# Kernel optimization log

Measured on AMD Instinct MI355X. Metric: run time of the kernel, lower is better.

The kernel has to match this reference:

```python
import jax, jax.numpy as jnp
import numpy as np

S, A, F, L, NCONV = 16, 512, 64, 12, 3


def setup_inputs() -> dict:
    key = jax.random.key(0)
    k1, k2, k3, k4 = jax.random.split(key, 4)
    node = jax.random.normal(k1, (S, A, F), dtype=jnp.float32)
    conn = jax.random.uniform(k2, (S, A, A, L), dtype=jnp.float32)
    bond = jax.random.normal(k3, (S, A, L, 2), dtype=jnp.float32)
    # filters.data.normal_() * (1/in_depth/1000) per ChemConv.__init__
    filters = jax.random.normal(k4, (NCONV, F, L, F + 2), dtype=jnp.float32) / (F * 1000.0)
    return {
        "node_property_tensor": node,
        "connectivity_tensor": conn,
        "bond_property_tensor": bond,
        "filters": filters,
    }


def _chemconv(x, conn, bond, w):
    # x: (S,A,F); conn: (S,A,A,L); bond: (S,A,L,2); w: (O,L,F+2)
    # gather neighbor features: bmm of (S,A,L,A) x (S,A,F) -> (S,A,L,F)
    ncv = jnp.einsum('sakl,skf->salf', conn, x)
    combined = jnp.concatenate([ncv, bond], axis=-1)  # (S,A,L,F+2)
    # elementwise-mul + double-sum == contraction over (L, F+2)
    return jnp.einsum('salc,olc->sao', combined, w)  # (S,A,O)


def reference(node_property_tensor, connectivity_tensor, bond_property_tensor, filters):
    out = node_property_tensor
    for i in range(filters.shape[0]):
        w = filters[i]  # same conv layer applied twice per residual pair
        out = jax.nn.relu(_chemconv(out, connectivity_tensor, bond_property_tensor, w))
        out = _chemconv(out, connectivity_tensor, bond_property_tensor, w)
        out = out + node_property_tensor  # residual to block input
        out = jax.nn.relu(out)
    return out
```

## Files before the change

kernel.cpp:

```cpp
#include <hip/hip_runtime.h>


typedef __attribute__((ext_vector_type(8))) short bf16x8;
typedef __attribute__((ext_vector_type(4))) float f32x4;
typedef unsigned short u16;
typedef unsigned int u32;
typedef unsigned char u8;
typedef long i64t;

#define YSCALE 16384.0f
#define YINV   (1.0f / 16384.0f)

__device__ __forceinline__ u16 f2bf(float f) {
  union { float f; u32 u; } x; x.f = f;
  u32 r = x.u + 0x7fffu + ((x.u >> 16) & 1u);
  return (u16)(r >> 16);
}

__device__ __forceinline__ u32 fp8pk4(float a, float b, float c, float d) {
  u32 w = __builtin_amdgcn_cvt_pk_fp8_f32(a, b, 0u, false);
  return __builtin_amdgcn_cvt_pk_fp8_f32(c, d, w, true);
}
__device__ __forceinline__ u32 fp8one(float v) {
  return __builtin_amdgcn_cvt_pk_fp8_f32(v, v, 0u, false) & 0xffu;
}

__device__ __forceinline__ void gload16(const void* g, void* l) {
  __builtin_amdgcn_global_load_lds((const __attribute__((address_space(1))) u32*)g,
                                   (__attribute__((address_space(3))) u32*)l, 16, 0, 0);
}

__global__ __launch_bounds__(256) void k_prep(const float* __restrict__ conn,
                                              const float* __restrict__ filters,
                                              const float* __restrict__ bond,
                                              u8* __restrict__ connQ,
                                              u16* __restrict__ wA,
                                              float* __restrict__ bW) {
  const int bid = blockIdx.x, tid = threadIdx.x;
  if (bid < 2048) {
    const unsigned n8 = 6291456u, stride = 2048 * 256;
    for (unsigned j = bid * 256 + tid; j < n8; j += stride) {
      const float4* s4 = (const float4*)conn;
      float4 a = s4[2 * (size_t)j], b = s4[2 * (size_t)j + 1];
      uint2 w;
      w.x = fp8pk4(a.x, a.y, a.z, a.w);
      w.y = fp8pk4(b.x, b.y, b.z, b.w);
      ((uint2*)connQ)[j] = w;
    }
  } else if (bid < 2624) {
    int t = (bid - 2048) * 256 + tid;
    int i = t / 49152;
    int rem = t - i * 49152;
    int row = rem >> 6, f = rem & 63;
    int l = row >> 6, o = row & 63;
    wA[t] = f2bf(filters[((size_t)((i * 64 + o) * 12 + l)) * 66 + f]);
  } else {
    __shared__ float wb[4608];
    __shared__ float lb[16 * 24];
    const int sa0 = (bid - 2624) * 16;
    for (int idx = tid; idx < 4608; idx += 256) {
      int i = idx / 1536, rem = idx - i * 1536;
      int o = rem / 24, lj = rem - o * 24;
      wb[idx] = filters[((size_t)((i * 64 + o) * 12 + (lj >> 1))) * 66 + 64 + (lj & 1)];
    }
    for (int t = tid; t < 384; t += 256)
      lb[t] = bond[(size_t)sa0 * 24 + t];
    __syncthreads();
#pragma unroll
    for (int it = 0; it < 12; ++it) {
      int idx = it * 256 + tid;
      int sl = idx / 192, rem = idx - sl * 192;
      int i = rem >> 6, o = rem & 63;
      float acc = 0.f;
#pragma unroll
      for (int lj = 0; lj < 24; ++lj)
        acc += lb[sl * 24 + lj] * wb[i * 1536 + o * 24 + lj];
      bW[(size_t)i * 524288 + (size_t)(sa0 + sl) * 64 + o] = acc;
    }
  }
}

__global__ __launch_bounds__(256) void k_yT(const float* __restrict__ node,
                                            const float* __restrict__ pOut,
                                            const float* __restrict__ bias,
                                            const u16* __restrict__ wAf,
                                            u8* __restrict__ yT,
                                            int mode, int addNode) {
  const int s = blockIdx.y, k0 = blockIdx.x * 32;
  __shared__ u16 xld[32 * 64];
  __shared__ u16 Z[12 * 64 * 36];
  const int tid = threadIdx.x, lane = tid & 63, wid = tid >> 6;
  const int r = lane & 15, g = lane >> 4;

  {
    const int row = tid >> 3, f0 = (tid & 7) * 8;
    const size_t e = ((size_t)(s * 512) + k0 + row) * 64 + f0;
    float v[8];
    if (mode == 0) {
      float4 a = *(const float4*)&node[e], b = *(const float4*)&node[e + 4];
      v[0] = a.x; v[1] = a.y; v[2] = a.z; v[3] = a.w;
      v[4] = b.x; v[5] = b.y; v[6] = b.z; v[7] = b.w;
    } else {
      float4 sa = {0, 0, 0, 0}, sb = {0, 0, 0, 0};
#pragma unroll
      for (int q = 0; q < 4; ++q) {
        float4 a = *(const float4*)&pOut[(size_t)q * 524288 + e];
        float4 b = *(const float4*)&pOut[(size_t)q * 524288 + e + 4];
        sa.x += a.x; sa.y += a.y; sa.z += a.z; sa.w += a.w;
        sb.x += b.x; sb.y += b.y; sb.z += b.z; sb.w += b.w;
      }
      float4 ba = *(const float4*)&bias[e], bb = *(const float4*)&bias[e + 4];
      sa.x = sa.x * YINV + ba.x; sa.y = sa.y * YINV + ba.y;
      sa.z = sa.z * YINV + ba.z; sa.w = sa.w * YINV + ba.w;
      sb.x = sb.x * YINV + bb.x; sb.y = sb.y * YINV + bb.y;
      sb.z = sb.z * YINV + bb.z; sb.w = sb.w * YINV + bb.w;
      if (addNode) {
        float4 na = *(const float4*)&node[e], nb = *(const float4*)&node[e + 4];
        sa.x += na.x; sa.y += na.y; sa.z += na.z; sa.w += na.w;
        sb.x += nb.x; sb.y += nb.y; sb.z += nb.z; sb.w += nb.w;
      }
      v[0] = fmaxf(sa.x, 0.f); v[1] = fmaxf(sa.y, 0.f);
      v[2] = fmaxf(sa.z, 0.f); v[3] = fmaxf(sa.w, 0.f);
      v[4] = fmaxf(sb.x, 0.f); v[5] = fmaxf(sb.y, 0.f);
      v[6] = fmaxf(sb.z, 0.f); v[7] = fmaxf(sb.w, 0.f);
    }
    ushort4 h0, h1;
    h0.x = f2bf(v[0]); h0.y = f2bf(v[1]); h0.z = f2bf(v[2]); h0.w = f2bf(v[3]);
    h1.x = f2bf(v[4]); h1.y = f2bf(v[5]); h1.z = f2bf(v[6]); h1.w = f2bf(v[7]);
    const int slot = (f0 >> 3) ^ (row & 7);
    *(ushort4*)&xld[row * 64 + slot * 8] = h0;
    *(ushort4*)&xld[row * 64 + slot * 8 + 4] = h1;
  }
  __syncthreads();

#pragma unroll
  for (int lw = 0; lw < 3; ++lw) {
    const int l = wid * 3 + lw;
    f32x4 acc[4][2] = {};
#pragma unroll
    for (int ks = 0; ks < 2; ++ks) {
      bf16x8 bv[2];
#pragma unroll
      for (int kt = 0; kt < 2; ++kt) {
        const int kk = kt * 16 + r;
        bv[kt] = *(const bf16x8*)&xld[kk * 64 + (((ks * 4 + g) ^ (kk & 7)) << 3)];
      }
#pragma unroll
      for (int ot = 0; ot < 4; ++ot) {
        bf16x8 av = *(const bf16x8*)&wAf[(size_t)(l * 64 + ot * 16 + r) * 64 + ks * 32 + g * 8];
#pragma unroll
        for (int kt = 0; kt < 2; ++kt)
          acc[ot][kt] = __builtin_amdgcn_mfma_f32_16x16x32_bf16(av, bv[kt], acc[ot][kt], 0, 0, 0);
      }
    }
#pragma unroll
    for (int ot = 0; ot < 4; ++ot)
#pragma unroll
      for (int kt = 0; kt < 2; ++kt)
#pragma unroll
        for (int r2 = 0; r2 < 4; ++r2) {
          int o = ot * 16 + g * 4 + r2, k = kt * 16 + r;
          Z[l * 2304 + o * 36 + k] = (u16)fp8one(acc[ot][kt][r2] * YSCALE);
        }
  }
  __syncthreads();
  u8* yb = yT + (size_t)s * 393216;
#pragma unroll
  for (int it = 0; it < 8; ++it) {
    int idx = it * 256 + tid;
    int o = idx >> 5, k = idx & 31;
    u32 b[12];
#pragma unroll
    for (int l = 0; l < 12; ++l) b[l] = (u32)(Z[l * 2304 + o * 36 + k] & 0xffu);
    u32* dst = (u32*)&yb[(size_t)o * 6144 + (size_t)(k0 + k) * 12];
    dst[0] = b[0] | (b[1] << 8) | (b[2] << 16) | (b[3] << 24);
    dst[1] = b[4] | (b[5] << 8) | (b[6] << 16) | (b[7] << 24);
    dst[2] = b[8] | (b[9] << 8) | (b[10] << 16) | (b[11] << 24);
  }
}

__global__ __launch_bounds__(512, 2) void k_stageB(const u8* __restrict__ connQ,
                                                   const u8* __restrict__ yT,
                                                   float* __restrict__ pOut) {
  const int b = blockIdx.x;
  const int s = (b & 7) * 2 + ((b >> 3) & 1);
  const int mt = (b >> 4) & 7, kq = b >> 7;
  const int row0 = mt * 64, k0 = kq * 1536;
  const u8* Ab = connQ + (size_t)(s * 512 + row0) * 6144 + k0;
  const u8* Bb = yT + (size_t)(s * 64) * 6144 + k0;
  __shared__ __align__(16) u8 lds[3 * 2 * 4096];
  const int tid = threadIdx.x, lane = tid & 63, wid = tid >> 6;
  const int r = lane & 15, g = lane >> 4;
  const int wr = wid & 3, wc = wid >> 2;
  const int isA = wid < 4;
  const int wseg = (isA ? wid : wid - 4) * 16;
  const u8* sbase = isA ? Ab : Bb;
  const int lrow = lane >> 2, lslot = lane & 3;
  const int side = isA ? 0 : 1;
  f32x4 acc[2] = {};

#define STAGE(T, NB)                                                            \
  {                                                                             \
    const int row = wseg + lrow;                                                \
    const int slot = lslot ^ ((row ^ (row >> 2)) & 3);                          \
    gload16(sbase + (size_t)row * 6144 + (size_t)(T) * 64 + slot * 16,          \
            &lds[((NB) * 2 + side) * 4096 + wseg * 64]);                        \
  }

  STAGE(0, 0);
  STAGE(1, 1);
  int nb = 0;
  for (int t = 0; t < 24; ++t) {
    if (t < 23) { asm volatile("s_waitcnt vmcnt(1)" ::: "memory"); }
    else        { asm volatile("s_waitcnt vmcnt(0)" ::: "memory"); }
    __builtin_amdgcn_s_barrier();
    if (t + 2 < 24) {
      int nb2 = nb + 2; if (nb2 >= 3) nb2 -= 3;
      STAGE(t + 2, nb2);
    }
    {
      const u8* bufA = &lds[(nb * 2 + 0) * 4096];
      const u8* bufB = &lds[(nb * 2 + 1) * 4096];
      const int arow = wr * 16 + r;
      const int ax = (arow ^ (arow >> 2)) & 3;
#pragma unroll
      for (int ks = 0; ks < 2; ++ks) {
        i64t av = *(const i64t*)&bufA[arow * 64 + (((ks * 2 + (g >> 1)) ^ ax) << 4) + ((g & 1) << 3)];
#pragma unroll
        for (int c = 0; c < 2; ++c) {
          const int col = wc * 32 + c * 16 + r;
          const int bx = (col ^ (col >> 2)) & 3;
          i64t bv = *(const i64t*)&bufB[col * 64 + (((ks * 2 + (g >> 1)) ^ bx) << 4) + ((g & 1) << 3)];
          acc[c] = __builtin_amdgcn_mfma_f32_16x16x32_fp8_fp8(av, bv, acc[c], 0, 0, 0);
        }
      }
    }
    if (++nb >= 3) nb -= 3;
  }
#undef STAGE
  float* po = pOut + (size_t)kq * 524288 + ((size_t)(s * 512) + row0) * 64;
#pragma unroll
  for (int c = 0; c < 2; ++c)
#pragma unroll
    for (int r2 = 0; r2 < 4; ++r2) {
      int m = wr * 16 + g * 4 + r2;
      int o = wc * 32 + c * 16 + r;
      po[m * 64 + o] = acc[c][r2];
    }
}

__global__ __launch_bounds__(256) void k_finalLast(const float* __restrict__ pOut,
                                                   const float* __restrict__ bW,
                                                   const float* __restrict__ node,
                                                   float* __restrict__ outF) {
  size_t e = ((size_t)blockIdx.x * 256 + threadIdx.x) * 4;
  float4 sv = {0, 0, 0, 0};
#pragma unroll
  for (int q = 0; q < 4; ++q) {
    float4 a = *(const float4*)&pOut[(size_t)q * 524288 + e];
    sv.x += a.x; sv.y += a.y; sv.z += a.z; sv.w += a.w;
  }
  float4 bw = *(const float4*)&bW[e];
  float4 nd = *(const float4*)&node[e];
  sv.x = fmaxf(sv.x * YINV + bw.x + nd.x, 0.f);
  sv.y = fmaxf(sv.y * YINV + bw.y + nd.y, 0.f);
  sv.z = fmaxf(sv.z * YINV + bw.z + nd.z, 0.f);
  sv.w = fmaxf(sv.w * YINV + bw.w + nd.w, 0.f);
  *(float4*)&outF[e] = sv;
}

__global__ __launch_bounds__(256) void k_fb_conv(const float* __restrict__ x,
                                                 const float* __restrict__ conn,
                                                 const float* __restrict__ bond,
                                                 const float* __restrict__ filt,
                                                 const float* __restrict__ node,
                                                 float* __restrict__ out, int addNode) {
  const int s = blockIdx.y, a = blockIdx.x;
  const int t = threadIdx.x;
  const int f = t & 63, lg = t >> 6;
  __shared__ float ncv[12 * 64];
  __shared__ float red[4][64];
  const float* cb = conn + ((size_t)(s * 512 + a)) * 6144;
  const float* xb = x + (size_t)s * 32768;
  float a0 = 0.f, a1 = 0.f, a2 = 0.f;
  for (int k = 0; k < 512; ++k) {
    float xv = xb[k * 64 + f];
    const float* cr = cb + k * 12 + lg * 3;
    a0 += cr[0] * xv; a1 += cr[1] * xv; a2 += cr[2] * xv;
  }
  ncv[(lg * 3 + 0) * 64 + f] = a0;
  ncv[(lg * 3 + 1) * 64 + f] = a1;
  ncv[(lg * 3 + 2) * 64 + f] = a2;
  __syncthreads();
  float p = 0.f;
  for (int l = lg * 3; l < lg * 3 + 3; ++l) {
    const float* wr = filt + ((size_t)(f * 12 + l)) * 66;
    float q = 0.f;
    for (int f2 = 0; f2 < 64; ++f2) q += ncv[l * 64 + f2] * wr[f2];
    q += bond[((size_t)(s * 512 + a) * 12 + l) * 2 + 0] * wr[64];
    q += bond[((size_t)(s * 512 + a) * 12 + l) * 2 + 1] * wr[65];
    p += q;
  }
  red[lg][f] = p;
  __syncthreads();
  if (t < 64) {
    float v = red[0][t] + red[1][t] + red[2][t] + red[3][t];
    if (addNode) v += node[((size_t)(s * 512 + a)) * 64 + t];
    out[((size_t)(s * 512 + a)) * 64 + t] = fmaxf(v, 0.f);
  }
}

extern "C" void kernel_launch(void* const* d_in, const int* in_sizes, int n_in,
                              void* d_out, int out_size, void* d_ws, size_t ws_size,
                              hipStream_t stream) {
  (void)in_sizes; (void)n_in; (void)out_size;
  const float* node    = (const float*)d_in[0];
  const float* conn    = (const float*)d_in[1];
  const float* bond    = (const float*)d_in[2];
  const float* filters = (const float*)d_in[3];
  float* outF = (float*)d_out;

  const size_t OFF_CONNQ = 0;
  const size_t OFF_YT    = 50331648;
  const size_t OFF_WA    = 56623104;
  const size_t OFF_BW    = 56918016;
  const size_t OFF_POUT  = 63209472;
  const size_t WS_NEED   = 71598080;

  if (ws_size >= WS_NEED) {
    unsigned char* ws = (unsigned char*)d_ws;
    u8*  connQ = (u8*)(ws + OFF_CONNQ);
    u8*  yT    = (u8*)(ws + OFF_YT);
    u16* wA    = (u16*)(ws + OFF_WA);
    float* bW  = (float*)(ws + OFF_BW);
    float* pO  = (float*)(ws + OFF_POUT);

    k_prep<<<dim3(3136), dim3(256), 0, stream>>>(conn, filters, bond, connQ, wA, bW);
    k_yT<<<dim3(16, 16), dim3(256), 0, stream>>>(node, pO, bW, wA, yT, 0, 0);
    for (int j = 0; j < 6; ++j) {
      k_stageB<<<dim3(512), dim3(512), 0, stream>>>(connQ, yT, pO);
      if (j < 5) {
        k_yT<<<dim3(16, 16), dim3(256), 0, stream>>>(node, pO,
                                                     bW + (size_t)(j >> 1) * 524288,
                                                     wA + (size_t)((j + 1) >> 1) * 49152,
                                                     yT, 1, j & 1);
      } else {
        k_finalLast<<<dim3(512), dim3(256), 0, stream>>>(pO, bW + (size_t)2 * 524288,
                                                         node, outF);
      }
    }
  } else {
    float* buf = (float*)d_ws;
    const float* xc = node;
    for (int j = 0; j < 6; ++j) {
      int i = j >> 1;
      float* dst = (j & 1) ? outF : buf;
      k_fb_conv<<<dim3(512, 16), dim3(256), 0, stream>>>(xc, conn, bond,
                                                         filters + (size_t)i * 50688,
                                                         node, dst, j & 1);
      xc = dst;
    }
  }
}
```

Baseline: 176.3 us.

## Fuse fp8 quantization of connectivity into first stageB GEMM pass

Moves the fp32-to-fp8 conversion of the connectivity tensor out of the prep kernel and into the first stageB launch. In that launch the A-side waves load fp32 tiles into registers, convert them, write them to LDS for the MFMA, and also store the fp8 copy to global memory for the later five launches. This removes a separate pass that wrote the 50MB fp8 buffer and then read it back, at the cost of a more complex register-staged pipeline in the first GEMM and higher register pressure.

```diff
diff --git a/kernel.cpp b/kernel.cpp
--- a/kernel.cpp
+++ b/kernel.cpp
@@ -30,25 +30,13 @@
                                    (__attribute__((address_space(3))) u32*)l, 16, 0, 0);
 }
 
-__global__ __launch_bounds__(256) void k_prep(const float* __restrict__ conn,
-                                              const float* __restrict__ filters,
+__global__ __launch_bounds__(256) void k_prep(const float* __restrict__ filters,
                                               const float* __restrict__ bond,
-                                              u8* __restrict__ connQ,
                                               u16* __restrict__ wA,
                                               float* __restrict__ bW) {
   const int bid = blockIdx.x, tid = threadIdx.x;
-  if (bid < 2048) {
-    const unsigned n8 = 6291456u, stride = 2048 * 256;
-    for (unsigned j = bid * 256 + tid; j < n8; j += stride) {
-      const float4* s4 = (const float4*)conn;
-      float4 a = s4[2 * (size_t)j], b = s4[2 * (size_t)j + 1];
-      uint2 w;
-      w.x = fp8pk4(a.x, a.y, a.z, a.w);
-      w.y = fp8pk4(b.x, b.y, b.z, b.w);
-      ((uint2*)connQ)[j] = w;
-    }
-  } else if (bid < 2624) {
-    int t = (bid - 2048) * 256 + tid;
+  if (bid < 576) {
+    int t = bid * 256 + tid;
     int i = t / 49152;
     int rem = t - i * 49152;
     int row = rem >> 6, f = rem & 63;
@@ -57,7 +45,7 @@
   } else {
     __shared__ float wb[4608];
     __shared__ float lb[16 * 24];
-    const int sa0 = (bid - 2624) * 16;
+    const int sa0 = (bid - 576) * 16;
     for (int idx = tid; idx < 4608; idx += 256) {
       int i = idx / 1536, rem = idx - i * 1536;
       int o = rem / 24, lj = rem - o * 24;
@@ -179,7 +167,9 @@
   }
 }
 
-__global__ __launch_bounds__(512, 2) void k_stageB(const u8* __restrict__ connQ,
+template <int CVT>
+__global__ __launch_bounds__(512, 2) void k_stageB(const float* __restrict__ connF,
+                                                   u8* __restrict__ connQ,
                                                    const u8* __restrict__ yT,
                                                    float* __restrict__ pOut) {
   const int b = blockIdx.x;
@@ -194,11 +184,45 @@
   const int wr = wid & 3, wc = wid >> 2;
   const int isA = wid < 4;
   const int wseg = (isA ? wid : wid - 4) * 16;
-  const u8* sbase = isA ? Ab : Bb;
   const int lrow = lane >> 2, lslot = lane & 3;
-  const int side = isA ? 0 : 1;
   f32x4 acc[2] = {};
 
+#define ASTAGE(T, NB)                                                           \
+  {                                                                             \
+    const int row = wseg + lrow;                                                \
+    const int slot = lslot ^ ((row ^ (row >> 2)) & 3);                          \
+    gload16(Ab + (size_t)row * 6144 + (size_t)(T) * 64 + slot * 16,             \
+            &lds[((NB) * 2 + 0) * 4096 + wseg * 64]);                           \
+  }
+#define BSTAGE(T, NB)                                                           \
+  {                                                                             \
+    const int row = wseg + lrow;                                                \
+    const int slot = lslot ^ ((row ^ (row >> 2)) & 3);                          \
+    gload16(Bb + (size_t)row * 6144 + (size_t)(T) * 64 + slot * 16,             \
+            &lds[((NB) * 2 + 1) * 4096 + wseg * 64]);                           \
+  }
+#define COMPUTE(NB)                                                             \
+  {                                                                             \
+    const u8* bufA = &lds[((NB) * 2 + 0) * 4096];                               \
+    const u8* bufB = &lds[((NB) * 2 + 1) * 4096];                               \
+    const int arow = wr * 16 + r;                                               \
+    const int ax = (arow ^ (arow >> 2)) & 3;                                    \
+    _Pragma("unroll")                                                           \
+    for (int ks = 0; ks < 2; ++ks) {                                            \
+      i64t av = *(const i64t*)&bufA[arow * 64 + (((ks * 2 + (g >> 1)) ^ ax) << 4) + ((g & 1) << 3)]; \
+      _Pragma("unroll")                                                         \
+      for (int c = 0; c < 2; ++c) {                                             \
+        const int col = wc * 32 + c * 16 + r;                                   \
+        const int bx = (col ^ (col >> 2)) & 3;                                  \
+        i64t bv = *(const i64t*)&bufB[col * 64 + (((ks * 2 + (g >> 1)) ^ bx) << 4) + ((g & 1) << 3)]; \
+        acc[c] = __builtin_amdgcn_mfma_f32_16x16x32_fp8_fp8(av, bv, acc[c], 0, 0, 0); \
+      }                                                                         \
+    }                                                                           \
+  }
+
+  if constexpr (!CVT) {
+    const int side = isA ? 0 : 1;
+    const u8* sbase = isA ? Ab : Bb;
 #define STAGE(T, NB)                                                            \
   {                                                                             \
     const int row = wseg + lrow;                                                \
@@ -206,38 +230,73 @@
     gload16(sbase + (size_t)row * 6144 + (size_t)(T) * 64 + slot * 16,          \
             &lds[((NB) * 2 + side) * 4096 + wseg * 64]);                        \
   }
-
-  STAGE(0, 0);
-  STAGE(1, 1);
-  int nb = 0;
-  for (int t = 0; t < 24; ++t) {
-    if (t < 23) { asm volatile("s_waitcnt vmcnt(1)" ::: "memory"); }
-    else        { asm volatile("s_waitcnt vmcnt(0)" ::: "memory"); }
-    __builtin_amdgcn_s_barrier();
-    if (t + 2 < 24) {
-      int nb2 = nb + 2; if (nb2 >= 3) nb2 -= 3;
-      STAGE(t + 2, nb2);
-    }
-    {
-      const u8* bufA = &lds[(nb * 2 + 0) * 4096];
-      const u8* bufB = &lds[(nb * 2 + 1) * 4096];
-      const int arow = wr * 16 + r;
-      const int ax = (arow ^ (arow >> 2)) & 3;
-#pragma unroll
-      for (int ks = 0; ks < 2; ++ks) {
-        i64t av = *(const i64t*)&bufA[arow * 64 + (((ks * 2 + (g >> 1)) ^ ax) << 4) + ((g & 1) << 3)];
-#pragma unroll
-        for (int c = 0; c < 2; ++c) {
-          const int col = wc * 32 + c * 16 + r;
-          const int bx = (col ^ (col >> 2)) & 3;
-          i64t bv = *(const i64t*)&bufB[col * 64 + (((ks * 2 + (g >> 1)) ^ bx) << 4) + ((g & 1) << 3)];
-          acc[c] = __builtin_amdgcn_mfma_f32_16x16x32_fp8_fp8(av, bv, acc[c], 0, 0, 0);
+    STAGE(0, 0);
+    STAGE(1, 1);
+    int nb = 0;
+    for (int t = 0; t < 24; ++t) {
+      if (t < 23) { asm volatile("s_waitcnt vmcnt(1)" ::: "memory"); }
+      else        { asm volatile("s_waitcnt vmcnt(0)" ::: "memory"); }
+      __builtin_amdgcn_s_barrier();
+      if (t + 2 < 24) {
+        int nb2 = nb + 2; if (nb2 >= 3) nb2 -= 3;
+        STAGE(t + 2, nb2);
+      }
+      COMPUTE(nb);
+      if (++nb >= 3) nb -= 3;
+    }
+#undef STAGE
+  } else {
+    const int grow = s * 512 + row0 + wseg + lrow;
+    const float* afp = connF + (size_t)grow * 6144 + k0 + lslot * 16;
+    u8* aqp = connQ + (size_t)grow * 6144 + k0 + lslot * 16;
+    float4 pa0[4], pa1[4];
+#define ALOADF(PA, T)                                                           \
+    { const float* p = afp + (size_t)(T) * 64;                                  \
+      PA[0] = *(const float4*)(p + 0);  PA[1] = *(const float4*)(p + 4);        \
+      PA[2] = *(const float4*)(p + 8);  PA[3] = *(const float4*)(p + 12); }
+#define ACVTW(PA, T, NB)                                                        \
+    { uint4 q;                                                                  \
+      q.x = fp8pk4(PA[0].x, PA[0].y, PA[0].z, PA[0].w);                         \
+      q.y = fp8pk4(PA[1].x, PA[1].y, PA[1].z, PA[1].w);                         \
+      q.z = fp8pk4(PA[2].x, PA[2].y, PA[2].z, PA[2].w);                         \
+      q.w = fp8pk4(PA[3].x, PA[3].y, PA[3].z, PA[3].w);                         \
+      const int row = wseg + lrow;                                              \
+      const int dslot = lslot ^ ((row ^ (row >> 2)) & 3);                       \
+      *(uint4*)&lds[((NB) * 2 + 0) * 4096 + row * 64 + dslot * 16] = q;         \
+      *(uint4*)(aqp + (size_t)(T) * 64) = q; }
+
+    if (isA) { ALOADF(pa0, 0); ALOADF(pa1, 1); ACVTW(pa0, 0, 0); ALOADF(pa0, 2); }
+    else     { BSTAGE(0, 0); BSTAGE(1, 1); }
+#pragma unroll
+    for (int t = 0; t < 24; ++t) {
+      if (isA) {
+        asm volatile("s_waitcnt lgkmcnt(0)" ::: "memory");
+      } else {
+        if (t < 23) asm volatile("s_waitcnt vmcnt(1)" ::: "memory");
+        else        asm volatile("s_waitcnt vmcnt(0)" ::: "memory");
+      }
+      __builtin_amdgcn_s_barrier();
+      if (isA) {
+        if (t < 23) {
+          if ((t + 1) & 1) { ACVTW(pa1, t + 1, (t + 1) % 3); }
+          else             { ACVTW(pa0, t + 1, (t + 1) % 3); }
+          if (t + 3 < 24) {
+            if ((t + 3) & 1) { ALOADF(pa1, t + 3); }
+            else             { ALOADF(pa0, t + 3); }
+          }
         }
-      }
-    }
-    if (++nb >= 3) nb -= 3;
-  }
-#undef STAGE
+      } else {
+        if (t + 2 < 24) BSTAGE(t + 2, (t + 2) % 3);
+      }
+      COMPUTE(t % 3);
+    }
+#undef ALOADF
+#undef ACVTW
+  }
+#undef ASTAGE
+#undef BSTAGE
+#undef COMPUTE
+
   float* po = pOut + (size_t)kq * 524288 + ((size_t)(s * 512) + row0) * 64;
 #pragma unroll
   for (int c = 0; c < 2; ++c)
@@ -335,10 +394,13 @@
     float* bW  = (float*)(ws + OFF_BW);
     float* pO  = (float*)(ws + OFF_POUT);
 
-    k_prep<<<dim3(3136), dim3(256), 0, stream>>>(conn, filters, bond, connQ, wA, bW);
+    k_prep<<<dim3(1088), dim3(256), 0, stream>>>(filters, bond, wA, bW);
     k_yT<<<dim3(16, 16), dim3(256), 0, stream>>>(node, pO, bW, wA, yT, 0, 0);
     for (int j = 0; j < 6; ++j) {
-      k_stageB<<<dim3(512), dim3(512), 0, stream>>>(connQ, yT, pO);
+      if (j == 0)
+        k_stageB<1><<<dim3(512), dim3(512), 0, stream>>>(conn, connQ, yT, pO);
+      else
+        k_stageB<0><<<dim3(512), dim3(512), 0, stream>>>(conn, connQ, yT, pO);
       if (j < 5) {
         k_yT<<<dim3(16, 16), dim3(256), 0, stream>>>(node, pO,
                                                      bW + (size_t)(j >> 1) * 524288,
```

New measurement: 176.3 us. Within noise of the previous version (-0.0%).
